# Kernel optimization log

Measured on AMD Instinct MI355X. Metric: run time of the kernel, lower is better.

## Reference

```python
import jax, jax.numpy as jnp
import numpy as np

B, N, C, K, TOPK = 16, 4096, 256, 8, 2
EPS = 1e-6
RATIO = 0.1      # gate_geno_ratio
TEMP = 1.0       # gate_temperature


def setup_inputs() -> dict:
    key = jax.random.key(0)
    ks = jax.random.split(key, 8)
    s = np.float32(1.0 / np.sqrt(C))  # ~xavier scale for C->C linears
    return {
        "tokens": jax.random.normal(ks[0], (B, N, C), jnp.float32),
        "geno_vec": jax.random.normal(ks[1], (B, C), jnp.float32),
        # gate params (gate_proj init std=0.001; gate_geno given small random instead of exact-zero init so it contributes)
        "Wg": jax.random.normal(ks[2], (K, C), jnp.float32) * 0.001,
        "bg": jnp.zeros((K,), jnp.float32),
        "Wgg": jax.random.normal(ks[3], (K, C), jnp.float32) * 0.001,
        "bgg": jnp.zeros((K,), jnp.float32),
        # per-expert 2-layer MLP params (dropout inactive in eval)
        "W1": jax.random.normal(ks[4], (K, C, C), jnp.float32) * s,
        "b1": jnp.zeros((K, C), jnp.float32),
        "W2": jax.random.normal(ks[5], (K, C, C), jnp.float32) * s,
        "b2": jnp.zeros((K, C), jnp.float32),
    }


def reference(tokens, geno_vec, Wg, bg, Wgg, bgg, W1, b1, W2, b2):
    # gate logits: [B,N,K]
    logits = jnp.einsum("bnc,kc->bnk", tokens, Wg) + bg
    logits = logits + RATIO * (geno_vec @ Wgg.T + bgg)[:, None, :]
    logits = logits / TEMP

    topv, topi = jax.lax.top_k(logits, TOPK)          # [B,N,TOPK]
    topw = jax.nn.softmax(topv, axis=-1)
    topw = jnp.maximum(topw, EPS)
    topw = topw / topw.sum(-1, keepdims=True)

    # dense gate weight matrix W: [B,N,K] (scatter of topw at topi; topk indices are distinct)
    hot = jax.nn.one_hot(topi, K, dtype=tokens.dtype)  # [B,N,TOPK,K]
    Wmat = (hot * topw[..., None]).sum(-2)             # [B,N,K]

    # load-balance loss on hard usage (detached in original)
    usage = jax.lax.stop_gradient(hot.sum(-2).mean((0, 1)))  # [K]
    lb_loss = (jnp.std(usage) / (usage.mean() + EPS)) ** 2

    mass_sum = Wmat.sum(axis=1)                        # [B,K]

    # per-expert MLP computed densely over all tokens; zero gate weight kills
    # non-routed tokens exactly (same math as gather->MLP->scatter-add)
    def expert_center(k):
        h = jax.nn.relu(tokens @ W1[k].T + b1[k])      # [B,N,C]
        out = h @ W2[k].T + b2[k]                      # [B,N,C]
        return jnp.einsum("bn,bnc->bc", Wmat[:, :, k], out)

    centers_sum = jnp.stack([expert_center(k) for k in range(K)], axis=1)  # [B,K,C]
    centers = centers_sum / jnp.maximum(mass_sum, EPS)[..., None]

    routing_confidence = (topv[:, :, 0] - topv[:, :, 1]).mean()
    return centers, lb_loss, routing_confidence
```

## Files before the change

kernel.cpp:

```cpp
#include <hip/hip_runtime.h>

#define B_ 16
#define N_ 4096
#define C_ 256
#define K_ 8
#define EPS 1e-6f
#define RATIO 0.1f

typedef float f32x4 __attribute__((ext_vector_type(4)));
typedef __bf16 bf16x8 __attribute__((ext_vector_type(8)));

__device__ inline unsigned short f2bf(float f){
  unsigned int u = __float_as_uint(f);
  u += 0x7FFFu + ((u >> 16) & 1u);
  return (unsigned short)(u >> 16);
}
__device__ inline float bf2f(unsigned short h){
  return __uint_as_float(((unsigned int)h) << 16);
}

union BFu { ushort4 u4[2]; bf16x8 v; };

__global__ __launch_bounds__(256) void kA_gate(
    const float* __restrict__ tokens, const float* __restrict__ geno,
    const float* __restrict__ Wg, const float* __restrict__ bg,
    const float* __restrict__ Wgg, const float* __restrict__ bgg,
    const float* __restrict__ W1,
    unsigned short* __restrict__ W1swz, unsigned short* __restrict__ tok_bf,
    uint2* __restrict__ tokexp, int* __restrict__ lcnt_blk,
    float* __restrict__ mass_blk, float* __restrict__ conf_blk)
{
  __shared__ float ls[64][9];
  __shared__ unsigned short wgh[4096], wgl[4096];
  __shared__ float bg_s[K_], gl_s[K_], mass_s[K_];
  __shared__ int lcnt[K_];
  __shared__ float cred[4];
  int tid = threadIdx.x, lane = tid & 63, wave = tid >> 6;
  int quad = lane >> 4, l16 = lane & 15;
  int blk = blockIdx.x;
  int b = blk >> 6;
  int tok0 = (blk & 63) * 64;

  if (tid < 64){
    int g = blk*64 + tid;
    int o = g << 3;
    int lane6 = (o >> 3) & 63;
    int s  = (o >> 9) & 7;
    int nt = (o >> 12) & 15;
    int k  = o >> 16;
    int q2 = lane6 >> 4, r16 = lane6 & 15;
    const float* src = W1 + (k << 16) + ((nt*16 + r16) << 8) + s*32 + q2*8;
    unsigned short* dst = W1swz + o;
    #pragma unroll
    for (int e = 0; e < 8; ++e) dst[e] = f2bf(src[e]);
  }
  {
    f32x4 wa = *(const f32x4*)(Wg + tid*8);
    f32x4 wb = *(const f32x4*)(Wg + tid*8 + 4);
    #pragma unroll
    for (int e = 0; e < 4; ++e){
      unsigned short h = f2bf(wa[e]);
      wgh[tid*8 + e] = h;  wgl[tid*8 + e] = f2bf(wa[e] - bf2f(h));
      unsigned short h2 = f2bf(wb[e]);
      wgh[tid*8 + 4 + e] = h2;  wgl[tid*8 + 4 + e] = f2bf(wb[e] - bf2f(h2));
      wgh[2048 + tid*8 + e] = 0;      wgl[2048 + tid*8 + e] = 0;
      wgh[2048 + tid*8 + 4 + e] = 0;  wgl[2048 + tid*8 + 4 + e] = 0;
    }
  }
  if (tid < K_){ bg_s[tid] = bg[tid]; mass_s[tid] = 0.f; lcnt[tid] = 0; }
  {
    int k = wave*2 + (lane >> 5);
    int hl = lane & 31;
    f32x4 a0 = *(const f32x4*)(geno + b*C_ + hl*8);
    f32x4 a1 = *(const f32x4*)(geno + b*C_ + hl*8 + 4);
    f32x4 w0v = *(const f32x4*)(Wgg + k*C_ + hl*8);
    f32x4 w1v = *(const f32x4*)(Wgg + k*C_ + hl*8 + 4);
    float p = a0[0]*w0v[0] + a0[1]*w0v[1] + a0[2]*w0v[2] + a0[3]*w0v[3]
            + a1[0]*w1v[0] + a1[1]*w1v[1] + a1[2]*w1v[2] + a1[3]*w1v[3];
    #pragma unroll
    for (int off = 16; off; off >>= 1) p += __shfl_xor(p, off);
    if (hl == 0) gl_s[k] = RATIO * (p + bgg[k]);
  }
  __syncthreads();

  {
    int trow = tok0 + wave*16 + l16;
    const float* xsrc = tokens + ((size_t)b*N_ + trow)*C_ + quad*8;
    unsigned short* bdst = tok_bf + (((size_t)(b*N_ + trow)) << 8) + quad*8;
    f32x4 xa[8], xb[8];
    #pragma unroll
    for (int s = 0; s < 8; ++s){
      xa[s] = *(const f32x4*)(xsrc + s*32);
      xb[s] = *(const f32x4*)(xsrc + s*32 + 4);
    }
    asm volatile("" : "+v"(xa[0]), "+v"(xa[1]), "+v"(xa[2]), "+v"(xa[3]),
                      "+v"(xa[4]), "+v"(xa[5]), "+v"(xa[6]), "+v"(xa[7]));
    asm volatile("" : "+v"(xb[0]), "+v"(xb[1]), "+v"(xb[2]), "+v"(xb[3]),
                      "+v"(xb[4]), "+v"(xb[5]), "+v"(xb[6]), "+v"(xb[7]));
    f32x4 acc; acc.x = 0.f; acc.y = 0.f; acc.z = 0.f; acc.w = 0.f;
    #pragma unroll
    for (int s = 0; s < 8; ++s){
      BFu hi, lo;
      hi.u4[0].x = f2bf(xa[s][0]); hi.u4[0].y = f2bf(xa[s][1]);
      hi.u4[0].z = f2bf(xa[s][2]); hi.u4[0].w = f2bf(xa[s][3]);
      hi.u4[1].x = f2bf(xb[s][0]); hi.u4[1].y = f2bf(xb[s][1]);
      hi.u4[1].z = f2bf(xb[s][2]); hi.u4[1].w = f2bf(xb[s][3]);
      lo.u4[0].x = f2bf(xa[s][0] - bf2f(hi.u4[0].x));
      lo.u4[0].y = f2bf(xa[s][1] - bf2f(hi.u4[0].y));
      lo.u4[0].z = f2bf(xa[s][2] - bf2f(hi.u4[0].z));
      lo.u4[0].w = f2bf(xa[s][3] - bf2f(hi.u4[0].w));
      lo.u4[1].x = f2bf(xb[s][0] - bf2f(hi.u4[1].x));
      lo.u4[1].y = f2bf(xb[s][1] - bf2f(hi.u4[1].y));
      lo.u4[1].z = f2bf(xb[s][2] - bf2f(hi.u4[1].z));
      lo.u4[1].w = f2bf(xb[s][3] - bf2f(hi.u4[1].w));
      *(ushort4*)(bdst + s*32)     = hi.u4[0];
      *(ushort4*)(bdst + s*32 + 4) = hi.u4[1];
      bf16x8 bhi = *(const bf16x8*)(wgh + l16*C_ + s*32 + quad*8);
      bf16x8 blo = *(const bf16x8*)(wgl + l16*C_ + s*32 + quad*8);
      acc = __builtin_amdgcn_mfma_f32_16x16x32_bf16(hi.v, bhi, acc, 0, 0, 0);
      acc = __builtin_amdgcn_mfma_f32_16x16x32_bf16(lo.v, bhi, acc, 0, 0, 0);
      acc = __builtin_amdgcn_mfma_f32_16x16x32_bf16(hi.v, blo, acc, 0, 0, 0);
    }
    if (l16 < K_){
      #pragma unroll
      for (int rr = 0; rr < 4; ++rr){
        int tl = wave*16 + quad*4 + rr;
        ls[tl][l16] = acc[rr] + bg_s[l16] + gl_s[l16];
      }
    }
  }
  __syncthreads();

  if (quad == 0){
    int t = (wave << 4) | l16;
    float v0 = -1e30f, v1 = -1e30f; int i0 = 0, i1 = 0;
    #pragma unroll
    for (int kk = 0; kk < K_; ++kk){
      float l = ls[t][kk];
      if (l > v0){ v1 = v0; i1 = i0; v0 = l; i0 = kk; }
      else if (l > v1){ v1 = l; i1 = kk; }
    }
    float e  = expf(v1 - v0);
    float w0 = 1.f / (1.f + e), w1 = e / (1.f + e);
    w0 = fmaxf(w0, EPS); w1 = fmaxf(w1, EPS);
    float inv = 1.f / (w0 + w1);
    w0 *= inv; w1 *= inv;
    int p0 = atomicAdd(&lcnt[i0], 1);
    int p1 = atomicAdd(&lcnt[i1], 1);
    atomicAdd(&mass_s[i0], w0);
    atomicAdd(&mass_s[i1], w1);
    tokexp[(size_t)b*N_ + tok0 + t] =
      make_uint2((unsigned)(i0 | (i1 << 4) | (p0 << 8) | (p1 << 16)),
                 __float_as_uint(w0));
    float ca = v0 - v1;
    #pragma unroll
    for (int off = 8; off; off >>= 1) ca += __shfl_down(ca, off);
    if (l16 == 0) cred[wave] = ca;
  }
  __syncthreads();
  if (tid < K_){
    lcnt_blk[blk*K_ + tid] = lcnt[tid];
    mass_blk[blk*K_ + tid] = mass_s[tid];
  }
  if (tid == 0) conf_blk[blk] = cred[0] + cred[1] + cred[2] + cred[3];
}

__global__ __launch_bounds__(256) void kP_prefix(
    const int* __restrict__ lcnt_blk, const float* __restrict__ mass_blk,
    const float* __restrict__ conf_blk, const uint2* __restrict__ tokexp,
    int* __restrict__ cnt, float* __restrict__ mass,
    float* __restrict__ conf_b, uint2* __restrict__ bwi)
{
  __shared__ int bp[64][K_];
  __shared__ int tot[K_];
  int b = blockIdx.x, tid = threadIdx.x, lane = tid & 63, wave = tid >> 6;
  if (wave == 0){
    #pragma unroll
    for (int k = 0; k < K_; ++k){
      int v = lcnt_blk[(b*64 + lane)*K_ + k];
      int ps = v;
      #pragma unroll
      for (int off = 1; off < 64; off <<= 1){
        int t = __shfl_up(ps, off);
        if (lane >= off) ps += t;
      }
      bp[lane][k] = ps - v;
      if (lane == 63) tot[k] = ps;
      float mv = mass_blk[(b*64 + lane)*K_ + k];
      #pragma unroll
      for (int off = 32; off; off >>= 1) mv += __shfl_xor(mv, off);
      if (lane == 0) mass[b*K_ + k] = mv;
    }
    float cv = conf_blk[b*64 + lane];
    #pragma unroll
    for (int off = 32; off; off >>= 1) cv += __shfl_xor(cv, off);
    if (lane == 0) conf_b[b] = cv;
  }
  __syncthreads();
  if (tid < K_) cnt[b*K_ + tid] = tot[tid];
  #pragma unroll 1
  for (int it = 0; it < 16; ++it){
    int n = it*256 + tid;
    uint2 te = tokexp[(size_t)b*N_ + n];
    int e0 = te.x & 15, e1 = (te.x >> 4) & 15;
    int p0 = (te.x >> 8) & 255, p1 = (te.x >> 16) & 255;
    int j = n >> 6;
    float w0 = __uint_as_float(te.y);
    float w1 = 1.f - w0;
    bwi[(size_t)(b*K_ + e0)*N_ + bp[j][e0] + p0] = make_uint2((unsigned)n, te.y);
    bwi[(size_t)(b*K_ + e1)*N_ + bp[j][e1] + p1] =
      make_uint2((unsigned)n, __float_as_uint(w1));
  }
}

#define K4_STAGE(T, REG) do {                                                  \
    _Pragma("unroll")                                                          \
    for (int i = 0; i < 2; ++i){                                               \
      int c16 = (T)*512 + i*256 + tid;                                         \
      __builtin_amdgcn_global_load_lds(                                        \
        (const __attribute__((address_space(1))) unsigned int*)(wsrc + c16*8), \
        (__attribute__((address_space(3))) unsigned int*)(&Bs[REG][0] + (i*256 + tid)*8), \
        16, 0, 0);                                                             \
    }                                                                          \
  } while(0)

__global__ __launch_bounds__(256, 5) void k4_expert(
    const unsigned short* __restrict__ tok_bf, const unsigned short* __restrict__ W1swz,
    const float* __restrict__ b1, const int* __restrict__ cnt,
    const uint2* __restrict__ bwi, float* __restrict__ gpart)
{
  __shared__ unsigned short Bs[3][4096];
  __shared__ float wtok[128];
  __shared__ float red[2][4][16];
  __shared__ int Pb[129];

  int tid = threadIdx.x, lane = tid & 63, wave = tid >> 6;
  int quad = lane >> 4, l16 = lane & 15;

  if (wave == 0){
    int b2i = lane << 1;
    int cA = (cnt[b2i] + 127) >> 7;
    int cB = (cnt[b2i + 1] + 127) >> 7;
    int s = cA + cB;
    int ps = s;
    #pragma unroll
    for (int off = 1; off < 64; off <<= 1){
      int t = __shfl_up(ps, off);
      if (lane >= off) ps += t;
    }
    Pb[b2i]     = ps - s;
    Pb[b2i + 1] = ps - cB;
    if (lane == 63) Pb[128] = ps;
  }
  __syncthreads();

  int T = Pb[128];
  int lin = blockIdx.x;
  int wq = (lin & 7) * 144 + (lin >> 3);
  if (wq >= T) return;
  int lo = 0, hi = 128;
  #pragma unroll
  for (int it = 0; it < 7; ++it){
    int mid = (lo + hi) >> 1;
    if (Pb[mid] <= wq) lo = mid; else hi = mid;
  }
  int bucket = lo;
  int chunk = wq - Pb[lo];
  int bat = bucket >> 3, k = bucket & 7;
  int M = cnt[bucket];
  int Mm1 = M - 1;
  size_t bwbase = (size_t)bucket * N_;

  const unsigned short* wsrc = W1swz + ((size_t)k << 16);

  K4_STAGE(0, 0);
  K4_STAGE(1, 1);

  if (tid < 128){
    int tn = chunk*128 + tid;
    uint2 e = bwi[bwbase + min(tn, Mm1)];
    wtok[tid] = (tn < M) ? __uint_as_float(e.y) : 0.f;
  }

  int r0 = chunk*128 + (wave << 4) + l16;
  uint2 ev0 = bwi[bwbase + min(r0, Mm1)];
  uint2 ev1 = bwi[bwbase + min(r0 + 64, Mm1)];
  int nn0 = (int)ev0.x, nn1 = (int)ev1.x;
  const unsigned short* p0 = tok_bf + (((size_t)((bat << 12) + nn0)) << 8) + (quad << 3);
  const unsigned short* p1 = tok_bf + (((size_t)((bat << 12) + nn1)) << 8) + (quad << 3);
  bf16x8 a0[8], a1[8];
  #pragma unroll
  for (int s = 0; s < 8; ++s){
    a0[s] = *(const bf16x8*)(p0 + s*32);
    a1[s] = *(const bf16x8*)(p1 + s*32);
  }

  float bias[16];
  #pragma unroll
  for (int p = 0; p < 16; ++p) bias[p] = b1[(k << 8) + (p << 4) + l16];

  float* gdst = gpart + (size_t)(((bucket << 5) + chunk) << 8);
  int wq4 = (wave << 4) + (quad << 2);

  #pragma unroll
  for (int p = 0; p < 16; ++p){
    if (p < 15) asm volatile("s_waitcnt vmcnt(2) lgkmcnt(0)" ::: "memory");
    else        asm volatile("s_waitcnt vmcnt(0) lgkmcnt(0)" ::: "memory");
    __builtin_amdgcn_s_barrier();

    if (p > 0 && tid < 16){
      int pb = (p - 1) & 1;
      float sv = red[pb][0][tid] + red[pb][1][tid]
               + red[pb][2][tid] + red[pb][3][tid];
      gdst[((p - 1) << 4) + tid] = sv;
    }
    if (p <= 13) K4_STAGE(p + 2, (p + 2) % 3);

    f32x4 acc0, acc1;
    acc0.x=0.f; acc0.y=0.f; acc0.z=0.f; acc0.w=0.f;
    acc1.x=0.f; acc1.y=0.f; acc1.z=0.f; acc1.w=0.f;
    #pragma unroll
    for (int s = 0; s < 8; ++s){
      bf16x8 bb = *(const bf16x8*)(&Bs[p % 3][0] + ((s*64 + lane) << 3));
      acc0 = __builtin_amdgcn_mfma_f32_16x16x32_bf16(a0[s], bb, acc0, 0, 0, 0);
      acc1 = __builtin_amdgcn_mfma_f32_16x16x32_bf16(a1[s], bb, acc1, 0, 0, 0);
    }
    float pt = 0.f;
    #pragma unroll
    for (int rr = 0; rr < 4; ++rr){
      float h0 = fmaxf(acc0[rr] + bias[p], 0.f);
      float h1 = fmaxf(acc1[rr] + bias[p], 0.f);
      pt += wtok[wq4 + rr] * h0 + wtok[64 + wq4 + rr] * h1;
    }
    pt += __shfl_down(pt, 32);
    pt += __shfl_down(pt, 16);
    if (lane < 16) red[p & 1][wave][lane] = pt;
  }
  asm volatile("s_waitcnt lgkmcnt(0)" ::: "memory");
  __builtin_amdgcn_s_barrier();
  if (tid < 16){
    float sv = red[1][0][tid] + red[1][1][tid] + red[1][2][tid] + red[1][3][tid];
    gdst[(15 << 4) + tid] = sv;
  }
}

__global__ __launch_bounds__(256) void k5_centers(
    const float* __restrict__ gpart, const int* __restrict__ cnt,
    const float* __restrict__ W2, const float* __restrict__ b2,
    const float* __restrict__ mass, const float* __restrict__ conf_b,
    float* __restrict__ out)
{
  __shared__ float gv[C_];
  int z = blockIdx.x, tid = threadIdx.x;
  int k = z & 7;
  int nch = (cnt[z] + 127) >> 7;
  float sv = 0.f;
  for (int c = 0; c < nch; ++c)
    sv += gpart[(size_t)((((z << 5) + c) << 8) + tid)];
  gv[tid] = sv;
  __syncthreads();
  float m = mass[z];
  float inv = 1.f / fmaxf(m, EPS);
  int tq = tid & 3, cb = tid >> 2;
  #pragma unroll 1
  for (int h = 0; h < 2; ++h){
    int c = (blockIdx.y*2 + h)*64 + cb;
    const float4* wrow = (const float4*)(W2 + ((((k << 8) + c)) << 8));
    float dot = 0.f;
    #pragma unroll
    for (int jj = 0; jj < 16; ++jj){
      float4 w4 = wrow[jj*4 + tq];
      float4 g4 = *(const float4*)&gv[(jj*4 + tq) * 4];
      dot += w4.x*g4.x + w4.y*g4.y + w4.z*g4.z + w4.w*g4.w;
    }
    dot += __shfl_xor(dot, 1);
    dot += __shfl_xor(dot, 2);
    if (tq == 0) out[z*C_ + c] = (dot + m * b2[k*C_ + c]) * inv;
  }
  if (z == 0 && blockIdx.y == 0 && tid == 0){
    float u[K_];
    #pragma unroll
    for (int kk = 0; kk < K_; ++kk) u[kk] = 0.f;
    for (int i = 0; i < B_*K_; ++i) u[i & 7] += (float)cnt[i];
    float mean = 0.f;
    #pragma unroll
    for (int kk = 0; kk < K_; ++kk){ u[kk] *= (1.f / (float)(B_*N_)); mean += u[kk]; }
    mean *= (1.f / K_);
    float var = 0.f;
    #pragma unroll
    for (int kk = 0; kk < K_; ++kk){ float d = u[kk] - mean; var += d*d; }
    var *= (1.f / K_);
    float denom = mean + EPS;
    float cs = 0.f;
    for (int i = 0; i < B_; ++i) cs += conf_b[i];
    out[B_*K_*C_]     = var / (denom * denom);
    out[B_*K_*C_ + 1] = cs / (float)(B_*N_);
  }
}

extern "C" void kernel_launch(void* const* d_in, const int* in_sizes, int n_in,
                              void* d_out, int out_size, void* d_ws, size_t ws_size,
                              hipStream_t stream)
{
  const float* tokens = (const float*)d_in[0];
  const float* geno   = (const float*)d_in[1];
  const float* Wg     = (const float*)d_in[2];
  const float* bg     = (const float*)d_in[3];
  const float* Wgg    = (const float*)d_in[4];
  const float* bgg    = (const float*)d_in[5];
  const float* W1     = (const float*)d_in[6];
  const float* b1     = (const float*)d_in[7];
  const float* W2     = (const float*)d_in[8];
  const float* b2     = (const float*)d_in[9];
  float* out = (float*)d_out;
  char* ws = (char*)d_ws;
  unsigned short* W1swz = (unsigned short*)(ws);
  uint2* tokexp   = (uint2*)(ws + 1048576);
  int*   lcnt_blk = (int*)  (ws + 1572864);
  float* mass_blk = (float*)(ws + 1605632);
  float* conf_blk = (float*)(ws + 1638400);
  float* conf_b   = (float*)(ws + 1642496);
  int*   cnt      = (int*)  (ws + 1642560);
  float* mass     = (float*)(ws + 1643072);
  uint2* bwi      = (uint2*)(ws + 1643584);
  unsigned short* tok_bf = (unsigned short*)(ws + 5837888);
  float* gpart    = (float*)(ws + 39392320);

  kA_gate<<<1024, 256, 0, stream>>>(tokens, geno, Wg, bg, Wgg, bgg, W1,
                                    W1swz, tok_bf, tokexp, lcnt_blk,
                                    mass_blk, conf_blk);
  kP_prefix<<<16, 256, 0, stream>>>(lcnt_blk, mass_blk, conf_blk, tokexp,
                                    cnt, mass, conf_b, bwi);
  k4_expert<<<1152, 256, 0, stream>>>(tok_bf, W1swz, b1, cnt, bwi, gpart);
  k5_centers<<<dim3(128, 2), 256, 0, stream>>>(gpart, cnt, W2, b2, mass,
                                               conf_b, out);
}
```

Baseline: 212.0 us.

## Deepen W1 LDS pipeline to four stages and remap blocks per XCD batch

Grows the LDS ring for W1 tiles from three to four buffers. The next tile's async global-to-LDS load is now issued before the wait/barrier, so two loads stay in flight while computing. Block-to-work mapping also changes: each XCD takes the work items of two specific batches (xcd and xcd+8) in turn, which should improve L2 locality of token and weight reads. The cost is more LDS per block and a lower occupancy hint (5 to 4 blocks), which may reduce latency hiding.

```diff
diff --git a/kernel.cpp b/kernel.cpp
--- a/kernel.cpp
+++ b/kernel.cpp
@@ -224,12 +224,12 @@
     }                                                                          \
   } while(0)
 
-__global__ __launch_bounds__(256, 5) void k4_expert(
+__global__ __launch_bounds__(256, 4) void k4_expert(
     const unsigned short* __restrict__ tok_bf, const unsigned short* __restrict__ W1swz,
     const float* __restrict__ b1, const int* __restrict__ cnt,
     const uint2* __restrict__ bwi, float* __restrict__ gpart)
 {
-  __shared__ unsigned short Bs[3][4096];
+  __shared__ unsigned short Bs[4][4096];
   __shared__ float wtok[128];
   __shared__ float red[2][4][16];
   __shared__ int Pb[129];
@@ -254,10 +254,19 @@
   }
   __syncthreads();
 
-  int T = Pb[128];
-  int lin = blockIdx.x;
-  int wq = (lin & 7) * 144 + (lin >> 3);
-  if (wq >= T) return;
+  int xcd = blockIdx.x & 7, slot = blockIdx.x >> 3;
+  int base0 = Pb[xcd << 3];
+  int L1 = Pb[(xcd << 3) + 8] - base0;
+  int wq;
+  if (slot < L1){
+    wq = base0 + slot;
+  } else {
+    int s2 = slot - L1;
+    int base1 = Pb[(xcd + 8) << 3];
+    int L2n = Pb[((xcd + 8) << 3) + 8] - base1;
+    if (s2 >= L2n) return;
+    wq = base1 + s2;
+  }
   int lo = 0, hi = 128;
   #pragma unroll
   for (int it = 0; it < 7; ++it){
@@ -304,8 +313,14 @@
 
   #pragma unroll
   for (int p = 0; p < 16; ++p){
-    if (p < 15) asm volatile("s_waitcnt vmcnt(2) lgkmcnt(0)" ::: "memory");
-    else        asm volatile("s_waitcnt vmcnt(0) lgkmcnt(0)" ::: "memory");
+    if (p < 14){
+      K4_STAGE(p + 2, (p + 2) & 3);
+      asm volatile("s_waitcnt vmcnt(4) lgkmcnt(0)" ::: "memory");
+    } else if (p == 14){
+      asm volatile("s_waitcnt vmcnt(2) lgkmcnt(0)" ::: "memory");
+    } else {
+      asm volatile("s_waitcnt vmcnt(0) lgkmcnt(0)" ::: "memory");
+    }
     __builtin_amdgcn_s_barrier();
 
     if (p > 0 && tid < 16){
@@ -314,14 +329,13 @@
                + red[pb][2][tid] + red[pb][3][tid];
       gdst[((p - 1) << 4) + tid] = sv;
     }
-    if (p <= 13) K4_STAGE(p + 2, (p + 2) % 3);
 
     f32x4 acc0, acc1;
     acc0.x=0.f; acc0.y=0.f; acc0.z=0.f; acc0.w=0.f;
     acc1.x=0.f; acc1.y=0.f; acc1.z=0.f; acc1.w=0.f;
     #pragma unroll
     for (int s = 0; s < 8; ++s){
-      bf16x8 bb = *(const bf16x8*)(&Bs[p % 3][0] + ((s*64 + lane) << 3));
+      bf16x8 bb = *(const bf16x8*)(&Bs[p & 3][0] + ((s*64 + lane) << 3));
       acc0 = __builtin_amdgcn_mfma_f32_16x16x32_bf16(a0[s], bb, acc0, 0, 0, 0);
       acc1 = __builtin_amdgcn_mfma_f32_16x16x32_bf16(a1[s], bb, acc1, 0, 0, 0);
     }
```

New measurement: 181.4 us. -14.4%, faster.
